# Kernel tuning notes

Measured on AMD Instinct MI355X. Metric: run time of the kernel, lower is better.

Reference implementation:

```python
import jax, jax.numpy as jnp
import numpy as np

H = 16  # n_heads


def setup_inputs() -> dict:
    key = jax.random.key(0)
    ks = jax.random.split(key, 11)
    B, S, D = 2, 2048, 1024
    def rn(k, shape, scale=1.0):
        return jax.random.normal(k, shape, dtype=jnp.float32) * scale
    w_scale = 1.0 / np.sqrt(D)
    return {
        "queries": rn(ks[0], (B, S, D)),
        "keys": rn(ks[1], (B, S, D)),
        "values": rn(ks[2], (B, S, D)),
        "Wq": rn(ks[3], (D, D), w_scale), "bq": rn(ks[4], (D,), 0.02),
        "Wk": rn(ks[5], (D, D), w_scale), "bk": rn(ks[6], (D,), 0.02),
        "Wv": rn(ks[7], (D, D), w_scale), "bv": rn(ks[8], (D,), 0.02),
        "Wo": rn(ks[9], (D, D), w_scale), "bo": rn(ks[10], (D,), 0.02),
    }


def _split_heads(x, h):
    # [B, S, D] -> [B, h, S, D/h]
    B, S, D = x.shape
    return x.reshape(B, S, h, D // h).transpose(0, 2, 1, 3)


def reference(queries, keys, values, Wq, bq, Wk, bk, Wv, bv, Wo, bo):
    B, S, D = queries.shape
    Q = _split_heads(queries @ Wq + bq, H)  # [B,h,S,dk]
    K = _split_heads(keys @ Wk + bk, H)
    V = _split_heads(values @ Wv + bv, H)
    # Faithful quirk: scale by sqrt(seq_len), not sqrt(d_k)
    factor = jnp.sqrt(jnp.asarray(S, dtype=Q.dtype))
    scores = jnp.einsum("bhqd,bhkd->bhqk", Q, K) / factor  # [B,h,S,S]
    weights = jax.nn.softmax(scores, axis=-1)
    attn = jnp.einsum("bhqk,bhkd->bhqd", weights, V)  # [B,h,S,dk]
    attn = attn.transpose(0, 2, 1, 3).reshape(B, S, D)  # [B,S,D]
    return attn @ Wo + bo
```

## Files before the change

### kernel.cpp

```cpp
#include <hip/hip_runtime.h>

typedef unsigned short ushort_t;
typedef unsigned int uint_t;
typedef __attribute__((ext_vector_type(8))) short short8;
typedef __attribute__((ext_vector_type(4))) float floatx4;

#define QSCALE 0.03187936f

__device__ __forceinline__ ushort_t f2bf(float f) {
    union { float f; uint_t u; } c; c.f = f;
    uint_t u = c.u;
    return (ushort_t)((u + 0x7fffu + ((u >> 16) & 1u)) >> 16);
}
__device__ __forceinline__ floatx4 mfma16x32(short8 a, short8 b, floatx4 c) {
    return __builtin_amdgcn_mfma_f32_16x16x32_bf16(a, b, c, 0, 0, 0);
}
__device__ __forceinline__ floatx4 zero4() { floatx4 z = {0.f, 0.f, 0.f, 0.f}; return z; }

__device__ __forceinline__ void gload16(const ushort_t* g, ushort_t* l) {
    __builtin_amdgcn_global_load_lds(
        (const __attribute__((address_space(1))) void*)g,
        (__attribute__((address_space(3))) void*)l, 16, 0, 0);
}

__global__ __launch_bounds__(256) void cvt_bf16(
    const float* __restrict__ s0, const float* __restrict__ s1,
    const float* __restrict__ s2, ushort_t* __restrict__ d0,
    ushort_t* __restrict__ d1, ushort_t* __restrict__ d2)
{
    const int which = blockIdx.x >> 11;
    const int blk = blockIdx.x & 2047;
    const float* src = (which == 0) ? s0 : (which == 1) ? s1 : s2;
    ushort_t* dst = (which == 0) ? d0 : (which == 1) ? d1 : d2;
    const int i = (blk * 256 + threadIdx.x) * 8;
    float4 f0 = *(const float4*)(src + i);
    float4 f1 = *(const float4*)(src + i + 4);
    __align__(16) ushort_t t[8];
    t[0] = f2bf(f0.x); t[1] = f2bf(f0.y); t[2] = f2bf(f0.z); t[3] = f2bf(f0.w);
    t[4] = f2bf(f1.x); t[5] = f2bf(f1.y); t[6] = f2bf(f1.z); t[7] = f2bf(f1.w);
    *(uint4*)(dst + i) = *(uint4*)t;
}

__global__ __launch_bounds__(256) void transpose_w(
    const float* __restrict__ W0, const float* __restrict__ W1,
    const float* __restrict__ W2, const float* __restrict__ W3,
    ushort_t* __restrict__ WT)
{
    __shared__ ushort_t tile[64][65];
    const float* W = (blockIdx.y == 0) ? W0 : (blockIdx.y == 1) ? W1
                   : (blockIdx.y == 2) ? W2 : W3;
    ushort_t* dst = WT + (size_t)blockIdx.y * (1024 * 1024);
    const int t = threadIdx.x;
    const int r = t >> 2, p = t & 3;
    const int j0 = (blockIdx.x & 15) << 6, k0 = (blockIdx.x >> 4) << 6;

    const float* src = W + (size_t)(k0 + r) * 1024 + j0 + p * 16;
    float4 f0 = *(const float4*)(src);
    float4 f1 = *(const float4*)(src + 4);
    float4 f2 = *(const float4*)(src + 8);
    float4 f3 = *(const float4*)(src + 12);
    ushort_t* tr = &tile[r][p * 16];
    tr[0] = f2bf(f0.x); tr[1] = f2bf(f0.y); tr[2]  = f2bf(f0.z); tr[3]  = f2bf(f0.w);
    tr[4] = f2bf(f1.x); tr[5] = f2bf(f1.y); tr[6]  = f2bf(f1.z); tr[7]  = f2bf(f1.w);
    tr[8] = f2bf(f2.x); tr[9] = f2bf(f2.y); tr[10] = f2bf(f2.z); tr[11] = f2bf(f2.w);
    tr[12] = f2bf(f3.x); tr[13] = f2bf(f3.y); tr[14] = f2bf(f3.z); tr[15] = f2bf(f3.w);
    __syncthreads();
    __align__(16) ushort_t buf[16];
#pragma unroll
    for (int i = 0; i < 16; ++i) buf[i] = tile[p * 16 + i][r];
    ushort_t* o = dst + (size_t)(j0 + r) * 1024 + k0 + p * 16;
    *(uint4*)(o)     = *(uint4*)(buf);
    *(uint4*)(o + 8) = *(uint4*)(buf + 8);
}

__global__ __launch_bounds__(256) void gemm_bt(
    const ushort_t* __restrict__ A0, const ushort_t* __restrict__ A1,
    const ushort_t* __restrict__ A2, const ushort_t* __restrict__ WT,
    const float* __restrict__ b0, const float* __restrict__ b1,
    const float* __restrict__ b2,
    ushort_t* __restrict__ Dq, ushort_t* __restrict__ Dk,
    ushort_t* __restrict__ Dv, int zbase)
{
    __shared__ __align__(16) ushort_t As[128 * 32];
    __shared__ __align__(16) ushort_t Bs[128 * 32];

    const int mode = blockIdx.z + zbase;
    const ushort_t* A = (mode == 0) ? A0 : (mode == 1) ? A1 : A2;
    const float* bias = (mode == 0) ? b0 : (mode == 1) ? b1 : b2;
    const ushort_t* Bt = WT + (size_t)mode * 1048576;

    const int tid = threadIdx.x;
    const int lane = tid & 63, wid = tid >> 6;
    const int quad = lane >> 4, l16 = lane & 15;
    const int wm = wid >> 1, wn = wid & 1;
    const int row0 = blockIdx.y << 7, col0 = blockIdx.x << 7;

    floatx4 acc[4][4];
#pragma unroll
    for (int i = 0; i < 4; ++i)
#pragma unroll
        for (int j = 0; j < 4; ++j) acc[i][j] = zero4();

    const int i0 = tid, i1 = 256 + tid;
    const int r0_ = i0 >> 2, c0_ = (i0 & 3) ^ (r0_ & 3);
    const int r1_ = i1 >> 2, c1_ = (i1 & 3) ^ (r1_ & 3);
    const ushort_t* gA0 = A  + (size_t)(row0 + r0_) * 1024 + c0_ * 8;
    const ushort_t* gA1 = A  + (size_t)(row0 + r1_) * 1024 + c1_ * 8;
    const ushort_t* gB0 = Bt + (size_t)(col0 + r0_) * 1024 + c0_ * 8;
    const ushort_t* gB1 = Bt + (size_t)(col0 + r1_) * 1024 + c1_ * 8;
    ushort_t* lA0 = As + i0 * 8;  ushort_t* lA1 = As + i1 * 8;
    ushort_t* lB0 = Bs + i0 * 8;  ushort_t* lB1 = Bs + i1 * 8;

    const int ra = wm * 64 + l16, rb = wn * 64 + l16;
    const int sa_off = (quad ^ (l16 & 3)) * 8;

    for (int k0 = 0; k0 < 1024; k0 += 32) {
        __syncthreads();
        gload16(gA0 + k0, lA0);
        gload16(gA1 + k0, lA1);
        gload16(gB0 + k0, lB0);
        gload16(gB1 + k0, lB1);
        __syncthreads();

        short8 af[4], bf[4];
#pragma unroll
        for (int i = 0; i < 4; ++i)
            af[i] = *(const short8*)(As + (ra + i * 16) * 32 + sa_off);
#pragma unroll
        for (int j = 0; j < 4; ++j)
            bf[j] = *(const short8*)(Bs + (rb + j * 16) * 32 + sa_off);
#pragma unroll
        for (int i = 0; i < 4; ++i)
#pragma unroll
            for (int j = 0; j < 4; ++j)
                acc[i][j] = mfma16x32(af[i], bf[j], acc[i][j]);
    }

    const float sc = (mode == 0) ? QSCALE : 1.f;
#pragma unroll
    for (int i = 0; i < 4; ++i) {
#pragma unroll
        for (int j = 0; j < 4; ++j) {
            const int c = col0 + wn * 64 + j * 16 + l16;
            const float bv = bias[c];
#pragma unroll
            for (int rr = 0; rr < 4; ++rr) {
                const int r = row0 + wm * 64 + i * 16 + quad * 4 + rr;
                const float v = (acc[i][j][rr] + bv) * sc;
                const int b = r >> 11, s = r & 2047, h = c >> 6, d = c & 63;
                if (mode <= 1) {
                    ushort_t* D = (mode == 0) ? Dq : Dk;
                    D[(((b * 16 + h) * 2048 + s) << 6) + d] = f2bf(v);
                } else {
                    Dv[(((b * 16 + h) * 64 + d) << 11) + s] = f2bf(v);
                }
            }
        }
    }
}

__global__ __launch_bounds__(256) void gemm64(
    const ushort_t* __restrict__ A, const ushort_t* __restrict__ Bt,
    const float* __restrict__ bias, float* __restrict__ Dout)
{
    __shared__ __align__(16) ushort_t As[64 * 32];
    __shared__ __align__(16) ushort_t Bs[128 * 32];
    const int tid = threadIdx.x;
    const int lane = tid & 63, wid = tid >> 6;
    const int quad = lane >> 4, l16 = lane & 15;
    const int wm = wid >> 1, wn = wid & 1;
    const int row0 = blockIdx.y << 6, col0 = blockIdx.x << 7;

    floatx4 acc[2][4];
#pragma unroll
    for (int i = 0; i < 2; ++i)
#pragma unroll
        for (int j = 0; j < 4; ++j) acc[i][j] = zero4();

    const int rA = tid >> 2, cA = (tid & 3) ^ (rA & 3);
    const ushort_t* gA = A + (size_t)(row0 + rA) * 1024 + cA * 8;
    ushort_t* lA = As + tid * 8;
    const int i0 = tid, i1 = 256 + tid;
    const int rB0 = i0 >> 2, cB0 = (i0 & 3) ^ (rB0 & 3);
    const int rB1 = i1 >> 2, cB1 = (i1 & 3) ^ (rB1 & 3);
    const ushort_t* gB0 = Bt + (size_t)(col0 + rB0) * 1024 + cB0 * 8;
    const ushort_t* gB1 = Bt + (size_t)(col0 + rB1) * 1024 + cB1 * 8;
    ushort_t* lB0 = Bs + i0 * 8;  ushort_t* lB1 = Bs + i1 * 8;

    const int sa_off = (quad ^ (l16 & 3)) * 8;

    for (int k0 = 0; k0 < 1024; k0 += 32) {
        __syncthreads();
        gload16(gA + k0, lA);
        gload16(gB0 + k0, lB0);
        gload16(gB1 + k0, lB1);
        __syncthreads();

        short8 af[2], bf[4];
#pragma unroll
        for (int i = 0; i < 2; ++i)
            af[i] = *(const short8*)(As + (wm * 32 + i * 16 + l16) * 32 + sa_off);
#pragma unroll
        for (int j = 0; j < 4; ++j)
            bf[j] = *(const short8*)(Bs + (wn * 64 + j * 16 + l16) * 32 + sa_off);
#pragma unroll
        for (int i = 0; i < 2; ++i)
#pragma unroll
            for (int j = 0; j < 4; ++j)
                acc[i][j] = mfma16x32(af[i], bf[j], acc[i][j]);
    }

#pragma unroll
    for (int i = 0; i < 2; ++i)
#pragma unroll
        for (int j = 0; j < 4; ++j) {
            const int c = col0 + wn * 64 + j * 16 + l16;
            const float bv = bias[c];
#pragma unroll
            for (int rr = 0; rr < 4; ++rr) {
                const int r = row0 + wm * 32 + i * 16 + quad * 4 + rr;
                Dout[(size_t)r * 1024 + c] = acc[i][j][rr] + bv;
            }
        }
}

__global__ __launch_bounds__(128, 2) void attn64q(
    const ushort_t* __restrict__ Q, const ushort_t* __restrict__ K,
    const ushort_t* __restrict__ Vt, ushort_t* __restrict__ Out)
{
    __shared__ __align__(16) ushort_t Ks[64 * 64];
    __shared__ __align__(16) ushort_t Vs[64 * 64];

    const int tid = threadIdx.x;
    const int lane = tid & 63, wid = tid >> 6;
    const int quad = lane >> 4, l16 = lane & 15;
    const int blk = blockIdx.x;
    const int bh = blk & 31;
    const int q0 = (blk >> 5) << 6;

    const ushort_t* Qh = Q + (size_t)bh * (2048 * 64);
    const ushort_t* Kh = K + (size_t)bh * (2048 * 64);
    const ushort_t* Vh = Vt + (size_t)bh * (64 * 2048);

    short8 qf0[2], qf1[2];
#pragma unroll
    for (int u = 0; u < 2; ++u) {
        const int qr = q0 + wid * 32 + u * 16 + l16;
        qf0[u] = *(const short8*)(Qh + (size_t)qr * 64 + quad * 8);
        qf1[u] = *(const short8*)(Qh + (size_t)qr * 64 + 32 + quad * 8);
    }

    float l_st[2] = {0.f, 0.f};
    floatx4 o_acc[2][4];
#pragma unroll
    for (int u = 0; u < 2; ++u)
#pragma unroll
        for (int d = 0; d < 4; ++d) o_acc[u][d] = zero4();

    const int kr = tid >> 3, kc = (tid & 7) ^ (kr & 7);
    const ushort_t* gK0 = Kh + (size_t)kr * 64 + kc * 8;
    const ushort_t* gV0 = Vh + (size_t)kr * 2048 + kc * 8;
    ushort_t* lK0 = Ks + tid * 8;
    ushort_t* lV0 = Vs + tid * 8;

    const int l7 = l16 & 7;
    const int q2 = quad >> 1, q1 = (quad & 1) * 4;

    for (int kt = 0; kt < 2048; kt += 64) {
        __syncthreads();
#pragma unroll
        for (int i = 0; i < 4; ++i) {
            gload16(gK0 + (size_t)kt * 64 + i * 1024, lK0 + i * 1024);
            gload16(gV0 + kt + (size_t)i * 32768, lV0 + i * 1024);
        }
        __syncthreads();

        floatx4 sa[2][4];
#pragma unroll
        for (int g = 0; g < 4; ++g) {
            const int row = g * 16 + l16;
            const short8 kf0 = *(const short8*)(Ks + row * 64 + ((quad ^ l7) * 8));
            const short8 kf1 = *(const short8*)(Ks + row * 64 + (((quad + 4) ^ l7) * 8));
#pragma unroll
            for (int u = 0; u < 2; ++u) {
                floatx4 t0 = mfma16x32(kf0, qf0[u], zero4());
                sa[u][g] = mfma16x32(kf1, qf1[u], t0);
            }
        }

#pragma unroll
        for (int G = 0; G < 2; ++G) {
            short8 pf[2];
#pragma unroll
            for (int u = 0; u < 2; ++u) {
                uint_t ub[8];
#pragma unroll
                for (int t = 0; t < 8; ++t) {
                    const int g = G * 2 + (t >> 2), r = t & 3;
                    const float e = __builtin_amdgcn_exp2f(fminf(sa[u][g][r], 80.f));
                    const uint_t uu = __float_as_uint(e) & 0xffff0000u;
                    l_st[u] += __uint_as_float(uu);
                    ub[t] = uu;
                }
                union { uint_t u4[4]; short8 s; } pc;
                pc.u4[0] = (ub[0] >> 16) | ub[1];
                pc.u4[1] = (ub[2] >> 16) | ub[3];
                pc.u4[2] = (ub[4] >> 16) | ub[5];
                pc.u4[3] = (ub[6] >> 16) | ub[7];
                pf[u] = pc.s;
            }
            const int ch0 = ((4 * G + q2) ^ l7) * 8;
            const int ch1 = ((4 * G + 2 + q2) ^ l7) * 8;
#pragma unroll
            for (int db = 0; db < 4; ++db) {
                const int vbase = (db * 16 + l16) * 64 + q1;
                const uint2 v0 = *(const uint2*)(Vs + vbase + ch0);
                const uint2 v1 = *(const uint2*)(Vs + vbase + ch1);
                union { uint_t u4[4]; short8 s; } vc;
                vc.u4[0] = v0.x; vc.u4[1] = v0.y; vc.u4[2] = v1.x; vc.u4[3] = v1.y;
                o_acc[0][db] = mfma16x32(pf[0], vc.s, o_acc[0][db]);
                o_acc[1][db] = mfma16x32(pf[1], vc.s, o_acc[1][db]);
            }
        }
    }

    const int b = bh >> 4, hh = bh & 15;
#pragma unroll
    for (int u = 0; u < 2; ++u) {
        float l = l_st[u];
        l += __shfl_xor(l, 16);
        l += __shfl_xor(l, 32);
        const int s0 = q0 + wid * 32 + u * 16 + quad * 4;
#pragma unroll
        for (int r = 0; r < 4; ++r) {
            const float lr = __shfl(l, quad * 4 + r);
            const float inv = 1.f / lr;
#pragma unroll
            for (int db = 0; db < 4; ++db) {
                const float v = o_acc[u][db][r] * inv;
                Out[(size_t)(b * 2048 + s0 + r) * 1024 + hh * 64 + db * 16 + l16] = f2bf(v);
            }
        }
    }
}

extern "C" void kernel_launch(void* const* d_in, const int* in_sizes, int n_in,
                              void* d_out, int out_size, void* d_ws, size_t ws_size,
                              hipStream_t stream) {
    const float* queries = (const float*)d_in[0];
    const float* keys    = (const float*)d_in[1];
    const float* values  = (const float*)d_in[2];
    const float* Wq = (const float*)d_in[3];
    const float* bq = (const float*)d_in[4];
    const float* Wk = (const float*)d_in[5];
    const float* bk = (const float*)d_in[6];
    const float* Wv = (const float*)d_in[7];
    const float* bv = (const float*)d_in[8];
    const float* Wo = (const float*)d_in[9];
    const float* bo = (const float*)d_in[10];
    float* out = (float*)d_out;

    char* ws = (char*)d_ws;
    const size_t MB = 1024 * 1024;
    ushort_t* WT = (ushort_t*)(ws);
    const ushort_t* WoT = WT + 3 * 1048576;
    dim3 tb(256);
    dim3 ta(128);

    transpose_w<<<dim3(256, 4), tb, 0, stream>>>(Wq, Wk, Wv, Wo, WT);

    if (ws_size >= 64 * MB) {
        ushort_t* Qb  = (ushort_t*)(ws + 8 * MB);
        ushort_t* Kb  = (ushort_t*)(ws + 16 * MB);
        ushort_t* Vb  = (ushort_t*)(ws + 24 * MB);
        ushort_t* Qp  = (ushort_t*)(ws + 32 * MB);
        ushort_t* Kp  = (ushort_t*)(ws + 40 * MB);
        ushort_t* Vtp = (ushort_t*)(ws + 48 * MB);
        ushort_t* An  = (ushort_t*)(ws + 56 * MB);
        cvt_bf16<<<dim3(6144), tb, 0, stream>>>(queries, keys, values, Qb, Kb, Vb);
        gemm_bt<<<dim3(8, 32, 3), tb, 0, stream>>>(Qb, Kb, Vb, WT,
            bq, bk, bv, Qp, Kp, Vtp, 0);
        attn64q<<<dim3(1024), ta, 0, stream>>>(Qp, Kp, Vtp, An);
        gemm64<<<dim3(8, 64), tb, 0, stream>>>(An, WoT, bo, out);
    } else {
        ushort_t* buf1 = (ushort_t*)(ws + 8 * MB);
        ushort_t* buf2 = (ushort_t*)(ws + 16 * MB);
        ushort_t* Qp   = (ushort_t*)(ws + 24 * MB);
        ushort_t* Kp   = (ushort_t*)(ws + 32 * MB);
        cvt_bf16<<<dim3(4096), tb, 0, stream>>>(queries, keys, keys, buf1, buf2, buf2);
        gemm_bt<<<dim3(8, 32, 2), tb, 0, stream>>>(buf1, buf2, buf2, WT,
            bq, bk, bk, Qp, Kp, Kp, 0);
        cvt_bf16<<<dim3(2048), tb, 0, stream>>>(values, values, values, buf1, buf1, buf1);
        gemm_bt<<<dim3(8, 32, 1), tb, 0, stream>>>(buf1, buf1, buf1, WT,
            bv, bv, bv, buf2, buf2, buf2, 2);
        attn64q<<<dim3(1024), ta, 0, stream>>>(Qp, Kp, buf2, buf1);
        gemm64<<<dim3(8, 64), tb, 0, stream>>>(buf1, WoT, bo, out);
    }
}
```

Before: 241.3 us.

## Double-buffer K/V tiles, use 4-wave blocks, and compute row sums via MFMA

The attention kernel now runs 256 threads per block covering 128 queries and double-buffers K/V tiles in LDS. The next tile's async load is issued before computing on the current one, so one barrier per iteration replaces two. The softmax denominator is accumulated with an MFMA against a ones vector instead of scalar adds and cross-lane shuffles. This doubles LDS use per block and may lower occupancy, and the sums now come from the bf16-rounded probabilities through the matrix unit.

```diff
diff --git a/kernel.cpp b/kernel.cpp
--- a/kernel.cpp
+++ b/kernel.cpp
@@ -224,19 +224,19 @@
         }
 }
 
-__global__ __launch_bounds__(128, 2) void attn64q(
+__global__ __launch_bounds__(256, 2) void attn64q(
     const ushort_t* __restrict__ Q, const ushort_t* __restrict__ K,
     const ushort_t* __restrict__ Vt, ushort_t* __restrict__ Out)
 {
-    __shared__ __align__(16) ushort_t Ks[64 * 64];
-    __shared__ __align__(16) ushort_t Vs[64 * 64];
+    __shared__ __align__(16) ushort_t Ks[2][64 * 64];
+    __shared__ __align__(16) ushort_t Vs[2][64 * 64];
 
     const int tid = threadIdx.x;
     const int lane = tid & 63, wid = tid >> 6;
     const int quad = lane >> 4, l16 = lane & 15;
     const int blk = blockIdx.x;
     const int bh = blk & 31;
-    const int q0 = (blk >> 5) << 6;
+    const int q0 = (blk >> 5) << 7;
 
     const ushort_t* Qh = Q + (size_t)bh * (2048 * 64);
     const ushort_t* Kh = K + (size_t)bh * (2048 * 64);
@@ -250,37 +250,49 @@
         qf1[u] = *(const short8*)(Qh + (size_t)qr * 64 + 32 + quad * 8);
     }
 
-    float l_st[2] = {0.f, 0.f};
-    floatx4 o_acc[2][4];
-#pragma unroll
-    for (int u = 0; u < 2; ++u)
+    floatx4 o_acc[2][4], lsum[2];
+#pragma unroll
+    for (int u = 0; u < 2; ++u) {
+        lsum[u] = zero4();
 #pragma unroll
         for (int d = 0; d < 4; ++d) o_acc[u][d] = zero4();
+    }
 
     const int kr = tid >> 3, kc = (tid & 7) ^ (kr & 7);
     const ushort_t* gK0 = Kh + (size_t)kr * 64 + kc * 8;
     const ushort_t* gV0 = Vh + (size_t)kr * 2048 + kc * 8;
-    ushort_t* lK0 = Ks + tid * 8;
-    ushort_t* lV0 = Vs + tid * 8;
+    ushort_t* lK0 = &Ks[0][0] + tid * 8;
+    ushort_t* lV0 = &Vs[0][0] + tid * 8;
 
     const int l7 = l16 & 7;
     const int q2 = quad >> 1, q1 = (quad & 1) * 4;
 
-    for (int kt = 0; kt < 2048; kt += 64) {
+    union { uint_t u4[4]; short8 s; } onep;
+    onep.u4[0] = onep.u4[1] = onep.u4[2] = onep.u4[3] = 0x3f803f80u;
+    const short8 ones = onep.s;
+
+#define STAGE(pp, kto) do {                                            \
+        gload16(gK0 + (size_t)(kto) * 64,         lK0 + (pp) * 4096);  \
+        gload16(gK0 + (size_t)(kto) * 64 + 2048,  lK0 + (pp) * 4096 + 2048); \
+        gload16(gV0 + (kto),                      lV0 + (pp) * 4096);  \
+        gload16(gV0 + (kto) + 65536,              lV0 + (pp) * 4096 + 2048); \
+    } while (0)
+
+    STAGE(0, 0);
+#pragma unroll 2
+    for (int it = 0; it < 32; ++it) {
+        const int p = it & 1;
         __syncthreads();
-#pragma unroll
-        for (int i = 0; i < 4; ++i) {
-            gload16(gK0 + (size_t)kt * 64 + i * 1024, lK0 + i * 1024);
-            gload16(gV0 + kt + (size_t)i * 32768, lV0 + i * 1024);
-        }
-        __syncthreads();
+        if (it < 31) STAGE(p ^ 1, (it + 1) * 64);
+        const ushort_t* ksp = &Ks[p][0];
+        const ushort_t* vsp = &Vs[p][0];
 
         floatx4 sa[2][4];
 #pragma unroll
         for (int g = 0; g < 4; ++g) {
             const int row = g * 16 + l16;
-            const short8 kf0 = *(const short8*)(Ks + row * 64 + ((quad ^ l7) * 8));
-            const short8 kf1 = *(const short8*)(Ks + row * 64 + (((quad + 4) ^ l7) * 8));
+            const short8 kf0 = *(const short8*)(ksp + row * 64 + ((quad ^ l7) * 8));
+            const short8 kf1 = *(const short8*)(ksp + row * 64 + (((quad + 4) ^ l7) * 8));
 #pragma unroll
             for (int u = 0; u < 2; ++u) {
                 floatx4 t0 = mfma16x32(kf0, qf0[u], zero4());
@@ -298,9 +310,7 @@
                 for (int t = 0; t < 8; ++t) {
                     const int g = G * 2 + (t >> 2), r = t & 3;
                     const float e = __builtin_amdgcn_exp2f(fminf(sa[u][g][r], 80.f));
-                    const uint_t uu = __float_as_uint(e) & 0xffff0000u;
-                    l_st[u] += __uint_as_float(uu);
-                    ub[t] = uu;
+                    ub[t] = __float_as_uint(e) & 0xffff0000u;
                 }
                 union { uint_t u4[4]; short8 s; } pc;
                 pc.u4[0] = (ub[0] >> 16) | ub[1];
@@ -308,14 +318,15 @@
                 pc.u4[2] = (ub[4] >> 16) | ub[5];
                 pc.u4[3] = (ub[6] >> 16) | ub[7];
                 pf[u] = pc.s;
+                lsum[u] = mfma16x32(pf[u], ones, lsum[u]);
             }
             const int ch0 = ((4 * G + q2) ^ l7) * 8;
             const int ch1 = ((4 * G + 2 + q2) ^ l7) * 8;
 #pragma unroll
             for (int db = 0; db < 4; ++db) {
                 const int vbase = (db * 16 + l16) * 64 + q1;
-                const uint2 v0 = *(const uint2*)(Vs + vbase + ch0);
-                const uint2 v1 = *(const uint2*)(Vs + vbase + ch1);
+                const uint2 v0 = *(const uint2*)(vsp + vbase + ch0);
+                const uint2 v1 = *(const uint2*)(vsp + vbase + ch1);
                 union { uint_t u4[4]; short8 s; } vc;
                 vc.u4[0] = v0.x; vc.u4[1] = v0.y; vc.u4[2] = v1.x; vc.u4[3] = v1.y;
                 o_acc[0][db] = mfma16x32(pf[0], vc.s, o_acc[0][db]);
@@ -323,18 +334,15 @@
             }
         }
     }
+#undef STAGE
 
     const int b = bh >> 4, hh = bh & 15;
 #pragma unroll
     for (int u = 0; u < 2; ++u) {
-        float l = l_st[u];
-        l += __shfl_xor(l, 16);
-        l += __shfl_xor(l, 32);
         const int s0 = q0 + wid * 32 + u * 16 + quad * 4;
 #pragma unroll
         for (int r = 0; r < 4; ++r) {
-            const float lr = __shfl(l, quad * 4 + r);
-            const float inv = 1.f / lr;
+            const float inv = 1.f / lsum[u][r];
 #pragma unroll
             for (int db = 0; db < 4; ++db) {
                 const float v = o_acc[u][db][r] * inv;
@@ -365,7 +373,6 @@
     ushort_t* WT = (ushort_t*)(ws);
     const ushort_t* WoT = WT + 3 * 1048576;
     dim3 tb(256);
-    dim3 ta(128);
 
     transpose_w<<<dim3(256, 4), tb, 0, stream>>>(Wq, Wk, Wv, Wo, WT);
 
@@ -380,7 +387,7 @@
         cvt_bf16<<<dim3(6144), tb, 0, stream>>>(queries, keys, values, Qb, Kb, Vb);
         gemm_bt<<<dim3(8, 32, 3), tb, 0, stream>>>(Qb, Kb, Vb, WT,
             bq, bk, bv, Qp, Kp, Vtp, 0);
-        attn64q<<<dim3(1024), ta, 0, stream>>>(Qp, Kp, Vtp, An);
+        attn64q<<<dim3(512), tb, 0, stream>>>(Qp, Kp, Vtp, An);
         gemm64<<<dim3(8, 64), tb, 0, stream>>>(An, WoT, bo, out);
     } else {
         ushort_t* buf1 = (ushort_t*)(ws + 8 * MB);
@@ -393,7 +400,7 @@
         cvt_bf16<<<dim3(2048), tb, 0, stream>>>(values, values, values, buf1, buf1, buf1);
         gemm_bt<<<dim3(8, 32, 1), tb, 0, stream>>>(buf1, buf1, buf1, WT,
             bv, bv, bv, buf2, buf2, buf2, 2);
-        attn64q<<<dim3(1024), ta, 0, stream>>>(Qp, Kp, buf2, buf1);
+        attn64q<<<dim3(512), tb, 0, stream>>>(Qp, Kp, buf2, buf1);
         gemm64<<<dim3(8, 64), tb, 0, stream>>>(buf1, WoT, bo, out);
     }
 }
```

After: 230.6 us. 1.05x faster.
